# Kernel tuning notes

Hardware: AMD Instinct MI355X
Metric: run time of the kernel (lower is better)

## Reference

```python
import jax, jax.numpy as jnp
import numpy as np

EPS_COS = 1e-8   # torch cosine_similarity eps
EPS_LN = 1e-5    # torch LayerNorm eps
SLOPE = 0.01     # torch LeakyReLU default negative_slope
N_HOP = 3
D_MODEL = 512
TEMP = 10.0


def _cos_sim(q, s):
    # q: [B, D], s: [B, S, D] -> [B, S]
    dot = jnp.einsum('bd,bsd->bs', q, s)
    qn = jnp.linalg.norm(q, axis=-1)          # [B]
    sn = jnp.linalg.norm(s, axis=-1)          # [B, S]
    return dot / jnp.maximum(qn[:, None] * sn, EPS_COS)


def _layer_norm(x, gamma, beta):
    mu = jnp.mean(x, axis=-1, keepdims=True)
    var = jnp.mean(jnp.square(x - mu), axis=-1, keepdims=True)
    return (x - mu) * jax.lax.rsqrt(var + EPS_LN) * gamma + beta


def setup_inputs() -> dict:
    key = jax.random.key(0)
    k1, k2, k3, k4 = jax.random.split(key, 4)
    B, S, D = 256, 512, D_MODEL
    query_emb = jax.random.normal(k1, (B, D), dtype=jnp.float32)
    state_emb = jax.random.normal(k2, (B, S, D), dtype=jnp.float32)
    # Stacked per-hop Linear params (txt branch), kaiming-uniform-ish scale
    lim = 1.0 / np.sqrt(D)
    W = jax.random.uniform(k3, (N_HOP, D, D), jnp.float32, -lim, lim)
    b = jax.random.uniform(k4, (N_HOP, D), jnp.float32, -lim, lim)
    ln_gamma = jnp.ones((D,), jnp.float32)
    ln_beta = jnp.zeros((D,), jnp.float32)
    return {"query_emb": query_emb, "state_emb": state_emb, "W": W, "b": b,
            "ln_gamma": ln_gamma, "ln_beta": ln_beta}


def reference(query_emb, state_emb, W, b, ln_gamma, ln_beta):
    q, s = query_emb, state_emb
    for i in range(N_HOP):
        dist = jax.nn.softmax(_cos_sim(q, s) * TEMP, axis=-1)       # [B, S]
        s = jax.nn.leaky_relu(jnp.einsum('bsd,de->bse', s, W[i].T) + b[i],
                              negative_slope=SLOPE)                  # [B, S, D]
        agg = jnp.einsum('bs,bsd->bd', dist, s)                      # [B, D]
        q = _layer_norm(q + agg, ln_gamma, ln_beta)
    final_dist = jax.nn.softmax(_cos_sim(q, s) * TEMP, axis=-1)
    return (q, final_dist)
```

## Files before the change

### kernel.cpp

```cpp
#include <hip/hip_runtime.h>
#include <hip/hip_bf16.h>
#include <stdint.h>

#define D 512
#define BATCH 256
#define SEQ 512

typedef __attribute__((ext_vector_type(8))) short short8;
typedef __attribute__((ext_vector_type(4))) float floatx4;

__device__ __forceinline__ float bf2f(unsigned short u) {
    union { unsigned int i; float f; } x; x.i = ((unsigned int)u) << 16; return x.f;
}
__device__ __forceinline__ unsigned short f2bf(float f) {
    union { float f; unsigned int i; } x; x.f = f;
    unsigned int i = x.i;
    unsigned int lsb = (i >> 16) & 1u;
    i += 0x7fffu + lsb;
    return (unsigned short)(i >> 16);
}

__device__ __forceinline__ float wred_sum(float v) {
    #pragma unroll
    for (int o = 32; o; o >>= 1) v += __shfl_xor(v, o, 64);
    return v;
}
__device__ __forceinline__ float gred_sum16(float v) {
    #pragma unroll
    for (int o = 8; o; o >>= 1) v += __shfl_xor(v, o, 64);
    return v;
}

__device__ __forceinline__ void llds16(const void* g, void* l) {
    auto gp = (const __attribute__((address_space(1))) void*)(g);
    auto lp = (__attribute__((address_space(3))) void*)(uintptr_t)(l);
    __builtin_amdgcn_global_load_lds(gp, lp, 16, 0, 0);
}

#define FENCE() asm volatile("" ::: "memory")
#define BARRIER() do { FENCE(); __builtin_amdgcn_s_barrier(); FENCE(); } while (0)

template<int WN>
__device__ __forceinline__ void waitvm() {
    if constexpr (WN == 6)      asm volatile("s_waitcnt vmcnt(6)" ::: "memory");
    else if constexpr (WN == 4) asm volatile("s_waitcnt vmcnt(4)" ::: "memory");
    else if constexpr (WN == 2) asm volatile("s_waitcnt vmcnt(2)" ::: "memory");
    else if constexpr (WN == 0) asm volatile("s_waitcnt vmcnt(0)" ::: "memory");
}

__global__ __launch_bounds__(1024)
void scores0_kernel(const float* __restrict__ state, const float* __restrict__ query,
                    float* __restrict__ dist_out, unsigned short* __restrict__ s_bf_out,
                    const float* __restrict__ W, unsigned short* __restrict__ Wb) {
    const int b = blockIdx.x, t = threadIdx.x, lane = t & 63, w = t >> 6;
    const int g = lane >> 4, ll = lane & 15;
    __shared__ float sc[SEQ];
    __shared__ float red[8];
    __shared__ float m_s, sum_s;

    {
        const int wi = b * 1024 + t;
        if (wi < 3 * D * D / 4) {
            float4 v = *(const float4*)(W + (size_t)wi * 4);
            ushort4 o;
            o.x = f2bf(v.x); o.y = f2bf(v.y); o.z = f2bf(v.z); o.w = f2bf(v.w);
            *(ushort4*)(Wb + (size_t)wi * 4) = o;
        }
    }

    float qv[4][8];
    {
        const float* qp = query + (size_t)b * D + ll * 8;
        #pragma unroll
        for (int j = 0; j < 4; ++j) {
            float4 a = *(const float4*)(qp + j * 128);
            float4 c = *(const float4*)(qp + j * 128 + 4);
            qv[j][0]=a.x; qv[j][1]=a.y; qv[j][2]=a.z; qv[j][3]=a.w;
            qv[j][4]=c.x; qv[j][5]=c.y; qv[j][6]=c.z; qv[j][7]=c.w;
        }
    }
    float qn2 = 0.f;
    #pragma unroll
    for (int j = 0; j < 4; ++j)
        #pragma unroll
        for (int e = 0; e < 8; ++e) qn2 += qv[j][e] * qv[j][e];
    const float qn = sqrtf(gred_sum16(qn2));

    const size_t bbase = (size_t)b * (SEQ * D);
    #pragma unroll 2
    for (int i = 0; i < 8; ++i) {
        const int row = w * 32 + i * 4 + g;
        const float* rp = state + bbase + (size_t)row * D + ll * 8;
        unsigned short* op = s_bf_out + bbase + (size_t)row * D + ll * 8;
        float dot = 0.f, nr = 0.f;
        #pragma unroll
        for (int j = 0; j < 4; ++j) {
            float4 a = *(const float4*)(rp + j * 128);
            float4 c = *(const float4*)(rp + j * 128 + 4);
            float v[8] = {a.x, a.y, a.z, a.w, c.x, c.y, c.z, c.w};
            short8 wv;
            #pragma unroll
            for (int e = 0; e < 8; ++e) wv[e] = (short)f2bf(v[e]);
            *(short8*)(op + j * 128) = wv;
            #pragma unroll
            for (int e = 0; e < 8; ++e) { dot += v[e] * qv[j][e]; nr += v[e] * v[e]; }
        }
        dot = gred_sum16(dot);
        nr  = gred_sum16(nr);
        if (ll == 0) sc[row] = 10.f * dot / fmaxf(qn * sqrtf(nr), 1e-8f);
    }
    __syncthreads();

    float sv = 0.f, ev = 0.f;
    if (t < 512) {
        sv = sc[t];
        float m = sv;
        #pragma unroll
        for (int o = 32; o; o >>= 1) m = fmaxf(m, __shfl_xor(m, o, 64));
        if (lane == 0) red[w] = m;
    }
    __syncthreads();
    if (t == 0) {
        float mm = red[0];
        #pragma unroll
        for (int k = 1; k < 8; ++k) mm = fmaxf(mm, red[k]);
        m_s = mm;
    }
    __syncthreads();
    if (t < 512) {
        ev = __expf(sv - m_s);
        float es = wred_sum(ev);
        if (lane == 0) red[w] = es;
    }
    __syncthreads();
    if (t == 0) {
        float s = 0.f;
        #pragma unroll
        for (int k = 0; k < 8; ++k) s += red[k];
        sum_s = s;
    }
    __syncthreads();
    if (t < 512) dist_out[b * SEQ + t] = ev / sum_s;
}

__global__ __launch_bounds__(1024)
void fused_kernel(const unsigned short* __restrict__ S, const float* __restrict__ part,
                  const float* __restrict__ q_in, const float* __restrict__ gamma,
                  const float* __restrict__ beta, float* __restrict__ q_out,
                  float* __restrict__ dist_out) {
    const int b = blockIdx.x, t = threadIdx.x, lane = t & 63, w = t >> 6;
    const int g = lane >> 4, ll = lane & 15;
    __shared__ float qs[D];
    __shared__ float sc[SEQ];
    __shared__ float red[8];
    __shared__ float mu_s, rstd_s, qn_s, m_s, sum_s;

    float x = 0.f;
    if (t < 512) {
        const float a = part[(size_t)b * D + t] + part[(size_t)(BATCH * D) + (size_t)b * D + t];
        x = q_in[(size_t)b * D + t] + a;
        float sm = wred_sum(x);
        if (lane == 0) red[w] = sm;
    }
    __syncthreads();
    if (t == 0) mu_s = (red[0]+red[1]+red[2]+red[3]+red[4]+red[5]+red[6]+red[7]) * (1.f / 512.f);
    __syncthreads();
    if (t < 512) {
        const float d = x - mu_s;
        float vv = wred_sum(d * d);
        if (lane == 0) red[w] = vv;
    }
    __syncthreads();
    if (t == 0) rstd_s = rsqrtf((red[0]+red[1]+red[2]+red[3]+red[4]+red[5]+red[6]+red[7]) * (1.f / 512.f) + 1e-5f);
    __syncthreads();
    if (t < 512) {
        const float y = (x - mu_s) * rstd_s * gamma[t] + beta[t];
        q_out[(size_t)b * D + t] = y;
        qs[t] = y;
        float s2 = wred_sum(y * y);
        if (lane == 0) red[w] = s2;
    }
    __syncthreads();
    if (t == 0) qn_s = sqrtf(red[0]+red[1]+red[2]+red[3]+red[4]+red[5]+red[6]+red[7]);
    __syncthreads();

    float qv[4][8];
    #pragma unroll
    for (int j = 0; j < 4; ++j) {
        float4 a = *(const float4*)&qs[j * 128 + ll * 8];
        float4 c = *(const float4*)&qs[j * 128 + ll * 8 + 4];
        qv[j][0]=a.x; qv[j][1]=a.y; qv[j][2]=a.z; qv[j][3]=a.w;
        qv[j][4]=c.x; qv[j][5]=c.y; qv[j][6]=c.z; qv[j][7]=c.w;
    }
    const float qn = qn_s;
    const size_t bbase = (size_t)b * (SEQ * D);
    #pragma unroll 2
    for (int i = 0; i < 8; ++i) {
        const int row = w * 32 + i * 4 + g;
        const unsigned short* rp = S + bbase + (size_t)row * D + ll * 8;
        float dot = 0.f, nr = 0.f;
        #pragma unroll
        for (int j = 0; j < 4; ++j) {
            short8 wv = *(const short8*)(rp + j * 128);
            #pragma unroll
            for (int e = 0; e < 8; ++e) {
                const float v = bf2f((unsigned short)wv[e]);
                dot += v * qv[j][e];
                nr += v * v;
            }
        }
        dot = gred_sum16(dot);
        nr  = gred_sum16(nr);
        if (ll == 0) sc[row] = 10.f * dot / fmaxf(qn * sqrtf(nr), 1e-8f);
    }
    __syncthreads();

    float sv = 0.f, ev = 0.f;
    if (t < 512) {
        sv = sc[t];
        float m = sv;
        #pragma unroll
        for (int o = 32; o; o >>= 1) m = fmaxf(m, __shfl_xor(m, o, 64));
        if (lane == 0) red[w] = m;
    }
    __syncthreads();
    if (t == 0) {
        float mm = red[0];
        #pragma unroll
        for (int k = 1; k < 8; ++k) mm = fmaxf(mm, red[k]);
        m_s = mm;
    }
    __syncthreads();
    if (t < 512) {
        ev = __expf(sv - m_s);
        float es = wred_sum(ev);
        if (lane == 0) red[w] = es;
    }
    __syncthreads();
    if (t == 0) {
        float s = 0.f;
        #pragma unroll
        for (int k = 0; k < 8; ++k) s += red[k];
        sum_s = s;
    }
    __syncthreads();
    if (t < 512) dist_out[b * SEQ + t] = ev / sum_s;
}

#define NKT 8

#define STA(BUF, H, KT) { const unsigned short* s_ = pA + (H) * 128 * D + (KT) * 64; \
    llds16(s_, &AsL[BUF][H][t * 8]); llds16(s_ + 64 * D, &AsL[BUF][H][t * 8 + 4096]); }
#define STB(BUF, H, KT) { const unsigned short* s_ = pB + (H) * 128 * D + (KT) * 64; \
    llds16(s_, &BsL[BUF][H][t * 8]); llds16(s_ + 64 * D, &BsL[BUF][H][t * 8 + 4096]); }

#define LDAF(BUF, MH) { _Pragma("unroll") for (int j = 0; j < 4; ++j) { \
    af[j][0] = *(const short8*)&AsL[BUF][MH][aoff[j] + xk0]; \
    af[j][1] = *(const short8*)&AsL[BUF][MH][aoff[j] + xk1]; } }
#define LDBF(BUF, NH) { _Pragma("unroll") for (int i = 0; i < 2; ++i) { \
    bfr[i][0] = *(const short8*)&BsL[BUF][NH][boff[i] + xk0]; \
    bfr[i][1] = *(const short8*)&BsL[BUF][NH][boff[i] + xk1]; } }

#define MMQ(MH, NH) { __builtin_amdgcn_s_setprio(1); \
    _Pragma("unroll") for (int kh = 0; kh < 2; ++kh) \
    _Pragma("unroll") for (int j = 0; j < 4; ++j) \
    _Pragma("unroll") for (int i = 0; i < 2; ++i) \
        acc[(MH) * 4 + j][(NH) * 2 + i] = __builtin_amdgcn_mfma_f32_16x16x32_bf16( \
            af[j][kh], bfr[i][kh], acc[(MH) * 4 + j][(NH) * 2 + i], 0, 0, 0); \
    __builtin_amdgcn_s_setprio(0); }

__global__ __launch_bounds__(512, 2)
void gemm_kernel(const unsigned short* __restrict__ A, const unsigned short* __restrict__ Bt,
                 const float* __restrict__ bias, const float* __restrict__ dist,
                 unsigned short* __restrict__ C, float* __restrict__ part) {
    __shared__ __align__(16) unsigned short AsL[2][2][128 * 64];
    __shared__ __align__(16) unsigned short BsL[2][2][128 * 64];
    __shared__ float dls[256];
    __shared__ float agg_lds[2][256];

    const int t = threadIdx.x, lane = t & 63, wid = t >> 6;
    const int wr = wid >> 2, wc = wid & 3;
    const int rr = lane & 15, lg = lane >> 4;
    const int bid = blockIdx.x;
    const int xcd = bid & 7, j8 = bid >> 3;
    const int nB = j8 & 1;
    const int mB = xcd * 64 + (j8 >> 1);
    const size_t tileM = (size_t)mB * 256;
    const int tileN = nB * 256;

    float b_r[4];
    #pragma unroll
    for (int ni = 0; ni < 4; ++ni) b_r[ni] = bias[tileN + (ni * 4 + wc) * 16 + rr];

    if (t < 128) {
        float2 v = *(const float2*)&dist[tileM + 2 * t];
        dls[2 * t] = v.x; dls[2 * t + 1] = v.y;
    }
    asm volatile("s_waitcnt lgkmcnt(0)" ::: "memory");

    const int srow = t >> 3, gc = (t & 7) ^ (srow & 7);
    const unsigned short* pA = A + (tileM + srow) * D + gc * 8;
    const unsigned short* pB = Bt + (size_t)(tileN + srow) * D + gc * 8;

    int aoff[4], boff[2];
    #pragma unroll
    for (int j = 0; j < 4; ++j) aoff[j] = ((j * 2 + wr) * 16 + rr) * 64;
    #pragma unroll
    for (int i = 0; i < 2; ++i) boff[i] = ((i * 4 + wc) * 16 + rr) * 64;
    const int xk0 = ((lg) ^ (rr & 7)) * 8;
    const int xk1 = ((4 + lg) ^ (rr & 7)) * 8;

    floatx4 acc[8][4];
    #pragma unroll
    for (int i = 0; i < 8; ++i)
        #pragma unroll
        for (int j = 0; j < 4; ++j) acc[i][j] = {0.f, 0.f, 0.f, 0.f};

    short8 af[4][2], bfr[2][2];

    STA(0, 0, 0); STB(0, 0, 0); STB(0, 1, 0); STA(0, 1, 0);

    for (int kt = 0; kt < NKT - 1; ++kt) {
        const int rb = kt & 1, sb = rb ^ 1, nk = kt + 1;
        STA(sb, 0, nk); waitvm<6>(); BARRIER();
        LDAF(rb, 0); LDBF(rb, 0); MMQ(0, 0); BARRIER();
        STB(sb, 0, nk); waitvm<6>(); BARRIER();
        LDBF(rb, 1); MMQ(0, 1); BARRIER();
        STB(sb, 1, nk); waitvm<6>(); BARRIER();
        LDAF(rb, 1); LDBF(rb, 0); MMQ(1, 0); BARRIER();
        STA(sb, 1, nk); BARRIER();
        LDBF(rb, 1); MMQ(1, 1); BARRIER();
    }
    {
        waitvm<4>(); BARRIER();
        LDAF(1, 0); LDBF(1, 0); MMQ(0, 0); BARRIER();
        waitvm<2>(); BARRIER();
        LDBF(1, 1); MMQ(0, 1); BARRIER();
        waitvm<0>(); BARRIER();
        LDAF(1, 1); LDBF(1, 0); MMQ(1, 0); BARRIER();
        LDBF(1, 1); MMQ(1, 1);
    }
    __syncthreads();

    float pacc[4] = {0.f, 0.f, 0.f, 0.f};
    #pragma unroll
    for (int mi = 0; mi < 8; ++mi) {
        const int rowb = (mi * 2 + wr) * 16 + lg * 4;
        const float4 dv = *(const float4*)&dls[rowb];
        #pragma unroll
        for (int ni = 0; ni < 4; ++ni) {
            const int col = tileN + (ni * 4 + wc) * 16 + rr;
            #pragma unroll
            for (int r2 = 0; r2 < 4; ++r2) {
                float v = acc[mi][ni][r2] + b_r[ni];
                v = v >= 0.f ? v : 0.01f * v;
                C[(tileM + rowb + r2) * D + col] = f2bf(v);
                pacc[ni] += (&dv.x)[r2] * v;
            }
        }
    }
    #pragma unroll
    for (int ni = 0; ni < 4; ++ni) {
        float p = pacc[ni];
        p += __shfl_xor(p, 16, 64);
        p += __shfl_xor(p, 32, 64);
        if (lg == 0) agg_lds[wr][(ni * 4 + wc) * 16 + rr] = p;
    }
    __syncthreads();
    if (t < 256) {
        const int b = mB >> 1;
        const float s = agg_lds[0][t] + agg_lds[1][t];
        part[(size_t)(mB & 1) * (BATCH * D) + (size_t)b * D + tileN + t] = s;
    }
}

extern "C" void kernel_launch(void* const* d_in, const int* in_sizes, int n_in,
                              void* d_out, int out_size, void* d_ws, size_t ws_size,
                              hipStream_t stream) {
    const float* query = (const float*)d_in[0];
    const float* state = (const float*)d_in[1];
    const float* W     = (const float*)d_in[2];
    const float* bias  = (const float*)d_in[3];
    const float* gamma = (const float*)d_in[4];
    const float* beta  = (const float*)d_in[5];

    float* out_q    = (float*)d_out;
    float* out_dist = (float*)d_out + BATCH * SEQ;

    char* ws = (char*)d_ws;
    const size_t SBYTES = (size_t)BATCH * SEQ * D * 2;
    unsigned short* sA = (unsigned short*)ws;
    unsigned short* sB = (unsigned short*)(ws + SBYTES);
    char* ext = ws + 2 * SBYTES;
    float* dist = (float*)ext;
    float* qbuf = (float*)(ext + 524288);
    float* part = (float*)(ext + 2 * 524288);
    unsigned short* Wb = (unsigned short*)(ext + 4 * 524288);

    dim3 ggrid(BATCH * SEQ / 256 * 2);

    scores0_kernel<<<BATCH, 1024, 0, stream>>>(state, query, dist, sA, W, Wb);
    gemm_kernel<<<ggrid, 512, 0, stream>>>(sA, Wb, bias, dist, sB, part);
    fused_kernel<<<BATCH, 1024, 0, stream>>>(sB, part, query, gamma, beta, qbuf, dist);
    gemm_kernel<<<ggrid, 512, 0, stream>>>(sB, Wb + D * D, bias + D, dist, sA, part);
    fused_kernel<<<BATCH, 1024, 0, stream>>>(sA, part, qbuf, gamma, beta, qbuf, dist);
    gemm_kernel<<<ggrid, 512, 0, stream>>>(sA, Wb + 2 * D * D, bias + 2 * D, dist, sB, part);
    fused_kernel<<<BATCH, 1024, 0, stream>>>(sB, part, qbuf, gamma, beta, out_q, out_dist);
}
```

Baseline: 421.8 us.

## Restructure GEMM mainloop into triple-buffered K=32 stages with one barrier per step

Replaces the double-buffered K=64 mainloop, which had eight barriers per iteration split across quadrant sub-steps, with a triple-buffered K=32 pipeline. Each step issues one barrier, prefetches the tile two steps ahead, loads the B fragments once and reuses them across both A halves. The LDS swizzle changes to a 4-chunk XOR pattern to match the narrower tile. LDS use drops from 128KB to 96KB, but there are twice as many K steps, and each barrier now has less MFMA work to hide behind.

New measurement: 441.5 us. 1.05x slower.

```diff
diff --git a/kernel.cpp b/kernel.cpp
--- a/kernel.cpp
+++ b/kernel.cpp
@@ -42,9 +42,7 @@
 
 template<int WN>
 __device__ __forceinline__ void waitvm() {
-    if constexpr (WN == 6)      asm volatile("s_waitcnt vmcnt(6)" ::: "memory");
-    else if constexpr (WN == 4) asm volatile("s_waitcnt vmcnt(4)" ::: "memory");
-    else if constexpr (WN == 2) asm volatile("s_waitcnt vmcnt(2)" ::: "memory");
+    if constexpr (WN == 4)      asm volatile("s_waitcnt vmcnt(4)" ::: "memory");
     else if constexpr (WN == 0) asm volatile("s_waitcnt vmcnt(0)" ::: "memory");
 }
 
@@ -247,34 +245,18 @@
     if (t < 512) dist_out[b * SEQ + t] = ev / sum_s;
 }
 
-#define NKT 8
-
-#define STA(BUF, H, KT) { const unsigned short* s_ = pA + (H) * 128 * D + (KT) * 64; \
-    llds16(s_, &AsL[BUF][H][t * 8]); llds16(s_ + 64 * D, &AsL[BUF][H][t * 8 + 4096]); }
-#define STB(BUF, H, KT) { const unsigned short* s_ = pB + (H) * 128 * D + (KT) * 64; \
-    llds16(s_, &BsL[BUF][H][t * 8]); llds16(s_ + 64 * D, &BsL[BUF][H][t * 8 + 4096]); }
-
-#define LDAF(BUF, MH) { _Pragma("unroll") for (int j = 0; j < 4; ++j) { \
-    af[j][0] = *(const short8*)&AsL[BUF][MH][aoff[j] + xk0]; \
-    af[j][1] = *(const short8*)&AsL[BUF][MH][aoff[j] + xk1]; } }
-#define LDBF(BUF, NH) { _Pragma("unroll") for (int i = 0; i < 2; ++i) { \
-    bfr[i][0] = *(const short8*)&BsL[BUF][NH][boff[i] + xk0]; \
-    bfr[i][1] = *(const short8*)&BsL[BUF][NH][boff[i] + xk1]; } }
-
-#define MMQ(MH, NH) { __builtin_amdgcn_s_setprio(1); \
-    _Pragma("unroll") for (int kh = 0; kh < 2; ++kh) \
-    _Pragma("unroll") for (int j = 0; j < 4; ++j) \
-    _Pragma("unroll") for (int i = 0; i < 2; ++i) \
-        acc[(MH) * 4 + j][(NH) * 2 + i] = __builtin_amdgcn_mfma_f32_16x16x32_bf16( \
-            af[j][kh], bfr[i][kh], acc[(MH) * 4 + j][(NH) * 2 + i], 0, 0, 0); \
-    __builtin_amdgcn_s_setprio(0); }
+#define STG(B3, KT) { \
+    llds16(pA + (KT) * 32,                    &AsL[B3][0][t * 8]); \
+    llds16(pB + (KT) * 32,                    &BsL[B3][0][t * 8]); \
+    llds16(pA + (size_t)128 * D + (KT) * 32,  &AsL[B3][1][t * 8]); \
+    llds16(pB + (size_t)128 * D + (KT) * 32,  &BsL[B3][1][t * 8]); }
 
 __global__ __launch_bounds__(512, 2)
 void gemm_kernel(const unsigned short* __restrict__ A, const unsigned short* __restrict__ Bt,
                  const float* __restrict__ bias, const float* __restrict__ dist,
                  unsigned short* __restrict__ C, float* __restrict__ part) {
-    __shared__ __align__(16) unsigned short AsL[2][2][128 * 64];
-    __shared__ __align__(16) unsigned short BsL[2][2][128 * 64];
+    __shared__ __align__(16) unsigned short AsL[3][2][128 * 32];
+    __shared__ __align__(16) unsigned short BsL[3][2][128 * 32];
     __shared__ float dls[256];
     __shared__ float agg_lds[2][256];
 
@@ -298,17 +280,16 @@
     }
     asm volatile("s_waitcnt lgkmcnt(0)" ::: "memory");
 
-    const int srow = t >> 3, gc = (t & 7) ^ (srow & 7);
+    const int srow = t >> 2, gc = (t & 3) ^ ((srow >> 1) & 3);
     const unsigned short* pA = A + (tileM + srow) * D + gc * 8;
     const unsigned short* pB = Bt + (size_t)(tileN + srow) * D + gc * 8;
 
-    int aoff[4], boff[2];
-    #pragma unroll
-    for (int j = 0; j < 4; ++j) aoff[j] = ((j * 2 + wr) * 16 + rr) * 64;
-    #pragma unroll
-    for (int i = 0; i < 2; ++i) boff[i] = ((i * 4 + wc) * 16 + rr) * 64;
-    const int xk0 = ((lg) ^ (rr & 7)) * 8;
-    const int xk1 = ((4 + lg) ^ (rr & 7)) * 8;
+    const int kx = (lg ^ ((rr >> 1) & 3)) * 8;
+    int arow[4], brow[4];
+    #pragma unroll
+    for (int j = 0; j < 4; ++j) arow[j] = ((j * 2 + wr) * 16 + rr) * 32 + kx;
+    #pragma unroll
+    for (int ni = 0; ni < 4; ++ni) brow[ni] = (((ni & 1) * 4 + wc) * 16 + rr) * 32 + kx;
 
     floatx4 acc[8][4];
     #pragma unroll
@@ -316,29 +297,36 @@
         #pragma unroll
         for (int j = 0; j < 4; ++j) acc[i][j] = {0.f, 0.f, 0.f, 0.f};
 
-    short8 af[4][2], bfr[2][2];
-
-    STA(0, 0, 0); STB(0, 0, 0); STB(0, 1, 0); STA(0, 1, 0);
-
-    for (int kt = 0; kt < NKT - 1; ++kt) {
-        const int rb = kt & 1, sb = rb ^ 1, nk = kt + 1;
-        STA(sb, 0, nk); waitvm<6>(); BARRIER();
-        LDAF(rb, 0); LDBF(rb, 0); MMQ(0, 0); BARRIER();
-        STB(sb, 0, nk); waitvm<6>(); BARRIER();
-        LDBF(rb, 1); MMQ(0, 1); BARRIER();
-        STB(sb, 1, nk); waitvm<6>(); BARRIER();
-        LDAF(rb, 1); LDBF(rb, 0); MMQ(1, 0); BARRIER();
-        STA(sb, 1, nk); BARRIER();
-        LDBF(rb, 1); MMQ(1, 1); BARRIER();
-    }
-    {
-        waitvm<4>(); BARRIER();
-        LDAF(1, 0); LDBF(1, 0); MMQ(0, 0); BARRIER();
-        waitvm<2>(); BARRIER();
-        LDBF(1, 1); MMQ(0, 1); BARRIER();
-        waitvm<0>(); BARRIER();
-        LDAF(1, 1); LDBF(1, 0); MMQ(1, 0); BARRIER();
-        LDBF(1, 1); MMQ(1, 1);
+    short8 af[4], bfr[4];
+
+    STG(0, 0); STG(1, 1);
+
+    #pragma unroll
+    for (int kt = 0; kt < 16; ++kt) {
+        const int b3 = kt % 3;
+        if (kt < 15) waitvm<4>(); else waitvm<0>();
+        BARRIER();
+        if (kt < 14) { STG((kt + 2) % 3, kt + 2); }
+        #pragma unroll
+        for (int j = 0; j < 4; ++j) af[j] = *(const short8*)&AsL[b3][0][arow[j]];
+        #pragma unroll
+        for (int ni = 0; ni < 4; ++ni) bfr[ni] = *(const short8*)&BsL[b3][ni >> 1][brow[ni]];
+        __builtin_amdgcn_s_setprio(1);
+        #pragma unroll
+        for (int j = 0; j < 4; ++j)
+            #pragma unroll
+            for (int ni = 0; ni < 4; ++ni)
+                acc[j][ni] = __builtin_amdgcn_mfma_f32_16x16x32_bf16(af[j], bfr[ni], acc[j][ni], 0, 0, 0);
+        __builtin_amdgcn_s_setprio(0);
+        #pragma unroll
+        for (int j = 0; j < 4; ++j) af[j] = *(const short8*)&AsL[b3][1][arow[j]];
+        __builtin_amdgcn_s_setprio(1);
+        #pragma unroll
+        for (int j = 0; j < 4; ++j)
+            #pragma unroll
+            for (int ni = 0; ni < 4; ++ni)
+                acc[4 + j][ni] = __builtin_amdgcn_mfma_f32_16x16x32_bf16(af[j], bfr[ni], acc[4 + j][ni], 0, 0, 0);
+        __builtin_amdgcn_s_setprio(0);
     }
     __syncthreads();
 
```

## Restructure GEMM main loop into two half-steps with full B fragments held

Applied to the files above, without the earlier changes.

The GEMM main loop is restructured from four quarter-steps per K tile, each with its own barriers and B-fragment reloads, into two half-steps. All four B fragments are loaded once per K tile and reused across both M halves. Prefetch issue points and vmcnt waits are regrouped to match. This cuts LDS reads of B and the barrier count per K tile, at the cost of more live registers for B fragments and coarser overlap between global loads and MFMA work.

After: 429.5 us. About the same (+1.8%).

```diff
diff --git a/kernel.cpp b/kernel.cpp
--- a/kernel.cpp
+++ b/kernel.cpp
@@ -42,9 +42,7 @@
 
 template<int WN>
 __device__ __forceinline__ void waitvm() {
-    if constexpr (WN == 6)      asm volatile("s_waitcnt vmcnt(6)" ::: "memory");
-    else if constexpr (WN == 4) asm volatile("s_waitcnt vmcnt(4)" ::: "memory");
-    else if constexpr (WN == 2) asm volatile("s_waitcnt vmcnt(2)" ::: "memory");
+    if constexpr (WN == 4)      asm volatile("s_waitcnt vmcnt(4)" ::: "memory");
     else if constexpr (WN == 0) asm volatile("s_waitcnt vmcnt(0)" ::: "memory");
 }
 
@@ -257,16 +255,16 @@
 #define LDAF(BUF, MH) { _Pragma("unroll") for (int j = 0; j < 4; ++j) { \
     af[j][0] = *(const short8*)&AsL[BUF][MH][aoff[j] + xk0]; \
     af[j][1] = *(const short8*)&AsL[BUF][MH][aoff[j] + xk1]; } }
-#define LDBF(BUF, NH) { _Pragma("unroll") for (int i = 0; i < 2; ++i) { \
-    bfr[i][0] = *(const short8*)&BsL[BUF][NH][boff[i] + xk0]; \
-    bfr[i][1] = *(const short8*)&BsL[BUF][NH][boff[i] + xk1]; } }
-
-#define MMQ(MH, NH) { __builtin_amdgcn_s_setprio(1); \
+#define LDBFALL(BUF) { _Pragma("unroll") for (int ni = 0; ni < 4; ++ni) { \
+    bfr[ni][0] = *(const short8*)&BsL[BUF][ni >> 1][boff[ni] + xk0]; \
+    bfr[ni][1] = *(const short8*)&BsL[BUF][ni >> 1][boff[ni] + xk1]; } }
+
+#define MMH(MH) { __builtin_amdgcn_s_setprio(1); \
     _Pragma("unroll") for (int kh = 0; kh < 2; ++kh) \
     _Pragma("unroll") for (int j = 0; j < 4; ++j) \
-    _Pragma("unroll") for (int i = 0; i < 2; ++i) \
-        acc[(MH) * 4 + j][(NH) * 2 + i] = __builtin_amdgcn_mfma_f32_16x16x32_bf16( \
-            af[j][kh], bfr[i][kh], acc[(MH) * 4 + j][(NH) * 2 + i], 0, 0, 0); \
+    _Pragma("unroll") for (int ni = 0; ni < 4; ++ni) \
+        acc[(MH) * 4 + j][ni] = __builtin_amdgcn_mfma_f32_16x16x32_bf16( \
+            af[j][kh], bfr[ni][kh], acc[(MH) * 4 + j][ni], 0, 0, 0); \
     __builtin_amdgcn_s_setprio(0); }
 
 __global__ __launch_bounds__(512, 2)
@@ -302,11 +300,11 @@
     const unsigned short* pA = A + (tileM + srow) * D + gc * 8;
     const unsigned short* pB = Bt + (size_t)(tileN + srow) * D + gc * 8;
 
-    int aoff[4], boff[2];
+    int aoff[4], boff[4];
     #pragma unroll
     for (int j = 0; j < 4; ++j) aoff[j] = ((j * 2 + wr) * 16 + rr) * 64;
     #pragma unroll
-    for (int i = 0; i < 2; ++i) boff[i] = ((i * 4 + wc) * 16 + rr) * 64;
+    for (int ni = 0; ni < 4; ++ni) boff[ni] = (((ni & 1) * 4 + wc) * 16 + rr) * 64;
     const int xk0 = ((lg) ^ (rr & 7)) * 8;
     const int xk1 = ((4 + lg) ^ (rr & 7)) * 8;
 
@@ -316,29 +314,22 @@
         #pragma unroll
         for (int j = 0; j < 4; ++j) acc[i][j] = {0.f, 0.f, 0.f, 0.f};
 
-    short8 af[4][2], bfr[2][2];
-
-    STA(0, 0, 0); STB(0, 0, 0); STB(0, 1, 0); STA(0, 1, 0);
-
-    for (int kt = 0; kt < NKT - 1; ++kt) {
-        const int rb = kt & 1, sb = rb ^ 1, nk = kt + 1;
-        STA(sb, 0, nk); waitvm<6>(); BARRIER();
-        LDAF(rb, 0); LDBF(rb, 0); MMQ(0, 0); BARRIER();
-        STB(sb, 0, nk); waitvm<6>(); BARRIER();
-        LDBF(rb, 1); MMQ(0, 1); BARRIER();
-        STB(sb, 1, nk); waitvm<6>(); BARRIER();
-        LDAF(rb, 1); LDBF(rb, 0); MMQ(1, 0); BARRIER();
-        STA(sb, 1, nk); BARRIER();
-        LDBF(rb, 1); MMQ(1, 1); BARRIER();
-    }
-    {
-        waitvm<4>(); BARRIER();
-        LDAF(1, 0); LDBF(1, 0); MMQ(0, 0); BARRIER();
-        waitvm<2>(); BARRIER();
-        LDBF(1, 1); MMQ(0, 1); BARRIER();
-        waitvm<0>(); BARRIER();
-        LDAF(1, 1); LDBF(1, 0); MMQ(1, 0); BARRIER();
-        LDBF(1, 1); MMQ(1, 1);
+    short8 af[4][2], bfr[4][2];
+
+    STA(0, 0, 0); STB(0, 0, 0); STA(0, 1, 0); STB(0, 1, 0);
+
+    for (int kt = 0; kt < NKT; ++kt) {
+        const int rb = kt & 1, sb = rb ^ 1;
+        if (kt < NKT - 1) { STA(sb, 0, kt + 1); STB(sb, 0, kt + 1); waitvm<4>(); }
+        else             { waitvm<0>(); }
+        BARRIER();
+        LDAF(rb, 0); LDBFALL(rb);
+        MMH(0);
+        BARRIER();
+        if (kt < NKT - 1) { STA(sb, 1, kt + 1); STB(sb, 1, kt + 1); }
+        LDAF(rb, 1);
+        MMH(1);
+        BARRIER();
     }
     __syncthreads();
 
```
